# Kernel tuning notes

Measured on AMD Instinct MI355X. Metric: run time of the kernel, lower is better.

## Reference

```python
import jax, jax.numpy as jnp
import numpy as np
from jax import lax

D_MODEL = 1024
D_STATE = 16
D_CONV = 4
D_INNER = 2048  # expand * d_model
DT_RANK = 64    # ceil(d_model / 16)
BATCH = 2
SEQ = 2048


def setup_inputs() -> dict:
    key = jax.random.key(0)
    ks = jax.random.split(key, 8)
    s = 0.02
    x = jax.random.normal(ks[0], (BATCH, SEQ, D_MODEL), jnp.float32)
    in_proj_w = jax.random.normal(ks[1], (2 * D_INNER, D_MODEL), jnp.float32) * s
    conv_w = jax.random.normal(ks[2], (D_INNER, 1, D_CONV), jnp.float32) * s  # [out, in/groups, k]
    conv_b = jax.random.normal(ks[3], (D_INNER,), jnp.float32) * s
    x_proj_w = jax.random.normal(ks[4], (DT_RANK + 2 * D_STATE, D_INNER), jnp.float32) * s
    dt_proj_w = jax.random.normal(ks[5], (D_INNER, DT_RANK), jnp.float32) * s
    dt_proj_b = jax.random.normal(ks[6], (D_INNER,), jnp.float32) * s
    A_log = jnp.log(jnp.tile(jnp.arange(1, D_STATE + 1, dtype=jnp.float32), (D_INNER, 1)))
    D = jnp.ones((D_INNER,), jnp.float32)
    out_proj_w = jax.random.normal(ks[7], (D_MODEL, D_INNER), jnp.float32) * s
    return dict(x=x, in_proj_w=in_proj_w, conv_w=conv_w, conv_b=conv_b,
                x_proj_w=x_proj_w, dt_proj_w=dt_proj_w, dt_proj_b=dt_proj_b,
                A_log=A_log, D=D, out_proj_w=out_proj_w)


def _causal_depthwise_conv(x_bcl, conv_w, conv_b):
    # x_bcl: [B, d_inner, L]; conv_w: [d_inner, 1, k]; left-pad k-1 -> causal, output length L
    y = lax.conv_general_dilated(
        x_bcl, conv_w,
        window_strides=(1,), padding=[(D_CONV - 1, 0)],
        feature_group_count=D_INNER,
        dimension_numbers=('NCH', 'OIH', 'NCH'))
    return y + conv_b[None, :, None]


def _ssm(xc, x_proj_w, dt_proj_w, dt_proj_b, A_log, D):
    # xc: [B, L, d_inner]
    A = -jnp.exp(A_log)                                   # [d, N]
    x_dbl = jnp.einsum('bld,rd->blr', xc, x_proj_w)       # [B, L, dt_rank + 2N]
    dt_low = x_dbl[..., :DT_RANK]
    Bm = x_dbl[..., DT_RANK:DT_RANK + D_STATE]            # [B, L, N]
    Cm = x_dbl[..., DT_RANK + D_STATE:]                   # [B, L, N]
    dt = jax.nn.softplus(jnp.einsum('blr,dr->bld', dt_low, dt_proj_w) + dt_proj_b)  # [B, L, d]
    dA = jnp.exp(dt[..., None] * A)                       # [B, L, d, N]
    dBx = dt[..., None] * Bm[:, :, None, :] * xc[..., None]  # [B, L, d, N]

    def step(h, inp):
        dA_t, dBx_t, C_t = inp                            # [B,d,N], [B,d,N], [B,N]
        h = dA_t * h + dBx_t
        y = jnp.einsum('bdn,bn->bd', h, C_t)
        return h, y

    h0 = jnp.zeros((xc.shape[0], D_INNER, D_STATE), xc.dtype)
    _, ys = lax.scan(step, h0,
                     (dA.transpose(1, 0, 2, 3), dBx.transpose(1, 0, 2, 3), Cm.transpose(1, 0, 2)))
    y = ys.transpose(1, 0, 2)                             # [B, L, d]
    return y + xc * D


def reference(x, in_proj_w, conv_w, conv_b, x_proj_w, dt_proj_w, dt_proj_b, A_log, D, out_proj_w):
    xz = jnp.einsum('blm,om->blo', x, in_proj_w)          # [B, L, 2*d_inner]
    xs, z = jnp.split(xz, 2, axis=-1)
    xc = _causal_depthwise_conv(xs.transpose(0, 2, 1), conv_w, conv_b).transpose(0, 2, 1)
    xc = jax.nn.silu(xc)
    y = _ssm(xc, x_proj_w, dt_proj_w, dt_proj_b, A_log, D)
    out = y * jax.nn.silu(z)
    return jnp.einsum('bld,md->blm', out, out_proj_w)
```

## Files before the change

### kernel.cpp

```cpp
#include <hip/hip_runtime.h>

#define SEQ    2048
#define DIN    2048
#define DMODEL 1024
#define NROWS  4096
#define NCH    64
#define CHL    32

typedef __attribute__((ext_vector_type(8))) _Float16 half8v;
typedef __attribute__((ext_vector_type(8))) unsigned short ushort8v;
typedef __attribute__((ext_vector_type(4))) float f32x4;

__device__ __forceinline__ float sigf(float x) { return 1.0f / (1.0f + __expf(-x)); }
__device__ __forceinline__ float softplusf(float v) {
    return fmaxf(v, 0.f) + __logf(1.f + __expf(-fabsf(v)));
}

__device__ __forceinline__ void gload16(const void* g, const void* l) {
    __builtin_amdgcn_global_load_lds((const __attribute__((address_space(1))) void*)g,
                                     (__attribute__((address_space(3))) void*)l, 16, 0, 0);
}

__device__ __forceinline__ unsigned short f2h(float x) {
    _Float16 h = (_Float16)x;
    unsigned short u;
    __builtin_memcpy(&u, &h, 2);
    return u;
}
__device__ __forceinline__ float h2f(unsigned short u) {
    _Float16 h;
    __builtin_memcpy(&h, &u, 2);
    return (float)h;
}

__global__ __launch_bounds__(256) void cvt_in_k(
    const float* __restrict__ x, const float* __restrict__ wi, const float* __restrict__ wx,
    const float* __restrict__ wd, const float* __restrict__ wo,
    unsigned short* __restrict__ xh, unsigned short* __restrict__ wih,
    unsigned short* __restrict__ wxh, unsigned short* __restrict__ wdh,
    unsigned short* __restrict__ woh)
{
    int i = blockIdx.x * 256 + threadIdx.x;
    if (i < 1048576) {
        float4 v = ((const float4*)x)[i];
        ushort4 h; h.x = f2h(v.x); h.y = f2h(v.y); h.z = f2h(v.z); h.w = f2h(v.w);
        ((ushort4*)xh)[i] = h;
    } else if (i < 2097152) {
        i -= 1048576;
        float4 v = ((const float4*)wi)[i];
        ushort4 h; h.x = f2h(v.x); h.y = f2h(v.y); h.z = f2h(v.z); h.w = f2h(v.w);
        ((ushort4*)wih)[i] = h;
    } else if (i < 2162688) {
        i -= 2097152;
        int row = i >> 9, q = i & 511;
        ushort4 h;
        if (row < 96) {
            float4 v = ((const float4*)wx)[(size_t)row * 512 + q];
            h.x = f2h(v.x); h.y = f2h(v.y); h.z = f2h(v.z); h.w = f2h(v.w);
        } else h = make_ushort4(0, 0, 0, 0);
        ((ushort4*)wxh)[(size_t)row * 512 + q] = h;
    } else if (i < 2195456) {
        i -= 2162688;
        float4 v = ((const float4*)wd)[i];
        ushort4 h; h.x = f2h(v.x); h.y = f2h(v.y); h.z = f2h(v.z); h.w = f2h(v.w);
        ((ushort4*)wdh)[i] = h;
    } else {
        i -= 2195456;
        float4 v = ((const float4*)wo)[i];
        ushort4 h; h.x = f2h(v.x); h.y = f2h(v.y); h.z = f2h(v.z); h.w = f2h(v.w);
        ((ushort4*)woh)[i] = h;
    }
}

__global__ __launch_bounds__(512, 4) void gemm_inproj(
    const unsigned short* __restrict__ A, const unsigned short* __restrict__ W,
    unsigned short* __restrict__ C, int K, int N, int mtiles, int lda, int ldw)
{
    __shared__ uint4 ldsu4[3072];
    char* lds = (char*)ldsu4;
    const int tid = threadIdx.x;
    const int w = tid >> 6, lane = tid & 63;

    const int nwg = gridDim.x;
    const int cpx = nwg >> 3;
    const int bid = blockIdx.x;
    const int swz = (bid & 7) * cpx + (bid >> 3);
    const int ntiles = nwg / mtiles;
    const int per = 8 * ntiles;
    const int gid = swz / per;
    const int rem = swz - gid * per;
    const int m0 = (gid * 8 + (rem & 7)) * 256;
    const int n0 = (rem >> 3) * 128;

    const int wr = w >> 2, wc = w & 3;
    const int lm = lane & 15, lk = lane >> 4;

    f32x4 acc[8][2];
#pragma unroll
    for (int i = 0; i < 8; ++i)
#pragma unroll
        for (int j = 0; j < 2; ++j) { acc[i][j][0]=0.f; acc[i][j][1]=0.f; acc[i][j][2]=0.f; acc[i][j][3]=0.f; }

    const int rsub = w * 8 + (lane >> 3);
    const int xr8  = ((lane & 7) ^ (lane >> 3)) << 3;
    const unsigned short* gA = A + (size_t)(m0 + rsub) * lda + xr8;
    const unsigned short* gW = W + (size_t)(n0 + rsub) * ldw + xr8;
    const int sdst = w * 1024;

    for (int kt = 0; kt < K; kt += 64) {
#pragma unroll
        for (int i = 0; i < 4; ++i)
            gload16(gA + (size_t)i * 64 * lda + kt, lds + i * 8192 + sdst);
#pragma unroll
        for (int i = 0; i < 2; ++i)
            gload16(gW + (size_t)i * 64 * ldw + kt, lds + 32768 + i * 8192 + sdst);
        __syncthreads();
#pragma unroll
        for (int kk = 0; kk < 2; ++kk) {
            half8v b[2];
#pragma unroll
            for (int nb = 0; nb < 2; ++nb) {
                const int br = wc * 32 + nb * 16 + lm;
                b[nb] = *(const half8v*)(lds + 32768 + br * 128 + (((kk * 4 + lk) ^ (br & 7)) << 4));
            }
            __builtin_amdgcn_s_setprio(1);
#pragma unroll
            for (int mb = 0; mb < 8; ++mb) {
                const int ar = wr * 128 + mb * 16 + lm;
                half8v a = *(const half8v*)(lds + ar * 128 + (((kk * 4 + lk) ^ (ar & 7)) << 4));
#pragma unroll
                for (int nb = 0; nb < 2; ++nb)
                    acc[mb][nb] = __builtin_amdgcn_mfma_f32_16x16x32_f16(a, b[nb], acc[mb][nb], 0, 0, 0);
            }
            __builtin_amdgcn_s_setprio(0);
        }
        __syncthreads();
    }

#pragma unroll
    for (int mb = 0; mb < 8; ++mb)
#pragma unroll
        for (int nb = 0; nb < 2; ++nb)
#pragma unroll
            for (int r = 0; r < 4; ++r)
                C[(size_t)(m0 + wr * 128 + mb * 16 + lk * 4 + r) * N + (n0 + wc * 32 + nb * 16 + lm)]
                    = f2h(acc[mb][nb][r]);
}

#define A_OFF 0
#define W_OFF 16384

__global__ __launch_bounds__(256) void gemm_mfma_h(
    const unsigned short* __restrict__ A, const unsigned short* __restrict__ W,
    unsigned short* __restrict__ C, int K, int ldc, int nmax, int mtiles,
    int sA1, int sA2, int ldw, const float* __restrict__ bias, int kspl, int cstride)
{
    __shared__ uint4 ldsu4[2048];
    char* lds = (char*)ldsu4;
    const int tid  = threadIdx.x;
    const int w    = tid >> 6, lane = tid & 63;

    const int nwg = gridDim.x;
    const int cpx = nwg >> 3;
    const int bid = blockIdx.x;
    const int swz = (bid & 7) * cpx + (bid >> 3);
    const int nbp = nwg / kspl;
    const int ks  = swz / nbp;
    const int tt  = swz - ks * nbp;
    const int ntiles = nbp / mtiles;
    const int per = 8 * ntiles;
    const int gid = tt / per;
    const int rem = tt - gid * per;
    const int m0 = (gid * 8 + (rem & 7)) * 128;
    const int n0 = (rem >> 3) * 128;
    const int kOff = ks * K;

    const int wr = w >> 1, wc = w & 1;

    f32x4 acc[4][4];
#pragma unroll
    for (int i = 0; i < 4; ++i)
#pragma unroll
        for (int j = 0; j < 4; ++j) { acc[i][j][0]=0.f; acc[i][j][1]=0.f; acc[i][j][2]=0.f; acc[i][j][3]=0.f; }

    const int rloc = w * 32 + (lane >> 3);
    const int xr8  = ((lane & 7) ^ (lane >> 3)) << 3;
    const int rowA = m0 + rloc;
    const unsigned short* gA = A + (size_t)(rowA >> 1) * sA2 + (size_t)(rowA & 1) * sA1 + kOff + xr8;
    const unsigned short* gW = W + (size_t)(n0 + rloc) * ldw + kOff + xr8;

    const int lm  = lane & 15;
    const int lk  = lane >> 4;
    const int lk4 = lk * 4;

    for (int kt = 0; kt < K; kt += 64) {
#pragma unroll
        for (int i = 0; i < 4; ++i) {
            const int rb = w * 32 + i * 8;
            gload16(gA + (size_t)i * 4 * sA2 + kt, lds + A_OFF + rb * 128);
            gload16(gW + (size_t)i * 8 * ldw + kt, lds + W_OFF + rb * 128);
        }
        __syncthreads();
#pragma unroll
        for (int h = 0; h < 2; ++h) {
            half8v af[4], wf[4];
            const int ch = h * 4 + lk;
#pragma unroll
            for (int t = 0; t < 4; ++t) {
                const int ar = wr * 64 + t * 16 + lm;
                const int wrw = wc * 64 + t * 16 + lm;
                af[t] = *(const half8v*)(lds + A_OFF + ar * 128 + ((ch ^ (ar & 7)) << 4));
                wf[t] = *(const half8v*)(lds + W_OFF + wrw * 128 + ((ch ^ (wrw & 7)) << 4));
            }
#pragma unroll
            for (int i = 0; i < 4; ++i)
#pragma unroll
                for (int j = 0; j < 4; ++j)
                    acc[i][j] = __builtin_amdgcn_mfma_f32_16x16x32_f16(af[i], wf[j], acc[i][j], 0, 0, 0);
        }
        __syncthreads();
    }

    unsigned short* Cp = C + (size_t)ks * cstride;
    if (bias) {
#pragma unroll
        for (int j = 0; j < 4; ++j) {
            const int n = n0 + wc * 64 + j * 16 + lm;
            const float bv = (n < nmax) ? bias[n] : 0.f;
#pragma unroll
            for (int i = 0; i < 4; ++i)
#pragma unroll
                for (int r = 0; r < 4; ++r) {
                    float v = acc[i][j][r] + bv;
                    if (n < nmax)
                        Cp[(size_t)(m0 + wr * 64 + i * 16 + lk4 + r) * ldc + n] = f2h(softplusf(v));
                }
        }
    } else {
#pragma unroll
        for (int i = 0; i < 4; ++i)
#pragma unroll
            for (int j = 0; j < 4; ++j) {
                const int n = n0 + wc * 64 + j * 16 + lm;
                if (n < nmax)
#pragma unroll
                    for (int r = 0; r < 4; ++r)
                        Cp[(size_t)(m0 + wr * 64 + i * 16 + lk4 + r) * ldc + n] = f2h(acc[i][j][r]);
            }
    }
}

__global__ __launch_bounds__(256) void xproj_reduce_k(
    const unsigned short* __restrict__ part, float* __restrict__ xdbl,
    unsigned short* __restrict__ dlh)
{
    int i = blockIdx.x * 256 + threadIdx.x;
    if (i >= NROWS * 32) return;
    int row = i >> 5, q = i & 31;
    float s0 = 0.f, s1 = 0.f, s2 = 0.f, s3 = 0.f;
#pragma unroll
    for (int ks = 0; ks < 8; ++ks) {
        ushort4 v = *(const ushort4*)(part + (size_t)ks * (NROWS * 128) + (size_t)row * 128 + q * 4);
        s0 += h2f(v.x); s1 += h2f(v.y); s2 += h2f(v.z); s3 += h2f(v.w);
    }
    if (q < 16) {
        ushort4 h; h.x = f2h(s0); h.y = f2h(s1); h.z = f2h(s2); h.w = f2h(s3);
        *(ushort4*)(dlh + (size_t)row * 64 + q * 4) = h;
    } else {
        *(float4*)(xdbl + (size_t)row * 96 + q * 4) = make_float4(s0, s1, s2, s3);
    }
}

__global__ __launch_bounds__(256) void out_reduce_k(
    const unsigned short* __restrict__ p, float* __restrict__ out)
{
    int i = blockIdx.x * 256 + threadIdx.x;
    ushort4 a = ((const ushort4*)p)[i];
    ushort4 b = ((const ushort4*)(p + 4194304))[i];
    float4 v;
    v.x = h2f(a.x) + h2f(b.x);
    v.y = h2f(a.y) + h2f(b.y);
    v.z = h2f(a.z) + h2f(b.z);
    v.w = h2f(a.w) + h2f(b.w);
    ((float4*)out)[i] = v;
}

__global__ __launch_bounds__(256) void conv_silu_k(
    const unsigned short* __restrict__ xzh, const float* __restrict__ cw,
    const float* __restrict__ cb, unsigned short* __restrict__ xch)
{
    int i = blockIdx.x * 256 + threadIdx.x;
    int d8 = (i & 255) << 3;
    int row = i >> 8;
    int l = row & (SEQ - 1);
    const unsigned short* base = xzh + (size_t)row * 4096 + d8;
    ushort8v x0 = *(const ushort8v*)base;
    ushort8v x1 = {}, x2 = {}, x3 = {};
    if (l >= 1) x1 = *(const ushort8v*)(base - 4096);
    if (l >= 2) x2 = *(const ushort8v*)(base - 8192);
    if (l >= 3) x3 = *(const ushort8v*)(base - 12288);
    ushort8v out;
#pragma unroll
    for (int j = 0; j < 8; ++j) {
        float4 wv = *(const float4*)(cw + (size_t)(d8 + j) * 4);
        float a = cb[d8 + j];
        a = fmaf(h2f(x3[j]), wv.x, a);
        a = fmaf(h2f(x2[j]), wv.y, a);
        a = fmaf(h2f(x1[j]), wv.z, a);
        a = fmaf(h2f(x0[j]), wv.w, a);
        out[j] = f2h(a * sigf(a));
    }
    *(ushort8v*)(xch + (size_t)row * DIN + d8) = out;
}

__global__ __launch_bounds__(256) void scan_pass1(
    const unsigned short* __restrict__ dth, const unsigned short* __restrict__ xch,
    const float* __restrict__ xdbl, const float* __restrict__ Alog,
    float* __restrict__ hbuf, float* __restrict__ apbuf)
{
    const int b = blockIdx.z, c = blockIdx.y;
    const int d = blockIdx.x * 256 + threadIdx.x;
    float A[16];
#pragma unroll
    for (int q = 0; q < 4; ++q) *(float4*)&A[q * 4] = *(const float4*)&Alog[(size_t)d * 16 + q * 4];
    bool seq = true;
#pragma unroll
    for (int n = 0; n < 16; ++n) {
        A[n] = -__expf(A[n]);
        seq = seq && (fabsf(A[n] + (float)(n + 1)) < 1e-5f * (float)(n + 1));
    }
    float h[16] = {};
    float sumdt = 0.f;
    const int rowbase = b * SEQ + c * CHL;
    int row = rowbase;
    float dtv = h2f(dth[(size_t)row * DIN + d]);
    float xcv = h2f(xch[(size_t)row * DIN + d]);
    if (seq) {
        for (int t = 0; t < CHL; ++t) {
            const int nrow = row + ((t + 1) < CHL ? 1 : 0);
            float dtv2 = h2f(dth[(size_t)nrow * DIN + d]);
            float xcv2 = h2f(xch[(size_t)nrow * DIN + d]);
            const float* xr = xdbl + (size_t)row * 96;
            float u = dtv * xcv;
            sumdt += dtv;
            float r = __expf(-dtv);
            float dA = r;
#pragma unroll
            for (int n = 0; n < 16; ++n) {
                h[n] = fmaf(dA, h[n], u * xr[64 + n]);
                dA *= r;
            }
            dtv = dtv2; xcv = xcv2; row = nrow;
        }
    } else {
        for (int t = 0; t < CHL; ++t) {
            const int nrow = row + ((t + 1) < CHL ? 1 : 0);
            float dtv2 = h2f(dth[(size_t)nrow * DIN + d]);
            float xcv2 = h2f(xch[(size_t)nrow * DIN + d]);
            const float* xr = xdbl + (size_t)row * 96;
            float u = dtv * xcv;
            sumdt += dtv;
#pragma unroll
            for (int n = 0; n < 16; ++n) {
                float dA = __expf(dtv * A[n]);
                h[n] = fmaf(dA, h[n], u * xr[64 + n]);
            }
            dtv = dtv2; xcv = xcv2; row = nrow;
        }
    }
    float ap[16];
    if (seq) {
        float R = __expf(-sumdt);
        float a = R;
#pragma unroll
        for (int n = 0; n < 16; ++n) { ap[n] = a; a *= R; }
    } else {
#pragma unroll
        for (int n = 0; n < 16; ++n) ap[n] = __expf(sumdt * A[n]);
    }
    size_t e = ((size_t)(b * NCH + c) << 15) + (size_t)d * 16;
#pragma unroll
    for (int q = 0; q < 4; ++q) {
        *(float4*)(hbuf + e + q * 4)  = *(float4*)&h[q * 4];
        *(float4*)(apbuf + e + q * 4) = *(float4*)&ap[q * 4];
    }
}

__global__ __launch_bounds__(256) void scan_pass2(
    float* __restrict__ hbuf, const float* __restrict__ apbuf)
{
    int idx = blockIdx.x * 256 + threadIdx.x;
    int b = idx >> 15;
    int dn = idx & 32767;
    float carry = 0.f;
    for (int c = 0; c < NCH; ++c) {
        size_t e = ((size_t)(b * NCH + c) << 15) + dn;
        float hl = hbuf[e];
        float ap = apbuf[e];
        hbuf[e] = carry;
        carry = fmaf(ap, carry, hl);
    }
}

__global__ __launch_bounds__(256) void scan_pass3(
    const unsigned short* __restrict__ dth, const unsigned short* __restrict__ xch,
    const unsigned short* __restrict__ xzh, const float* __restrict__ xdbl,
    const float* __restrict__ Alog, const float* __restrict__ Dp,
    const float* __restrict__ hbuf, unsigned short* __restrict__ oph)
{
    const int b = blockIdx.z, c = blockIdx.y;
    const int d = blockIdx.x * 256 + threadIdx.x;
    float A[16];
#pragma unroll
    for (int q = 0; q < 4; ++q) *(float4*)&A[q * 4] = *(const float4*)&Alog[(size_t)d * 16 + q * 4];
    bool seq = true;
#pragma unroll
    for (int n = 0; n < 16; ++n) {
        A[n] = -__expf(A[n]);
        seq = seq && (fabsf(A[n] + (float)(n + 1)) < 1e-5f * (float)(n + 1));
    }
    float h[16];
    size_t e = ((size_t)(b * NCH + c) << 15) + (size_t)d * 16;
#pragma unroll
    for (int q = 0; q < 4; ++q) *(float4*)&h[q * 4] = *(const float4*)(hbuf + e + q * 4);
    const float Dd = Dp[d];
    const int rowbase = b * SEQ + c * CHL;
    int row = rowbase;
    float dtv = h2f(dth[(size_t)row * DIN + d]);
    float xcv = h2f(xch[(size_t)row * DIN + d]);
    float zv  = h2f(xzh[(size_t)row * 4096 + DIN + d]);
    if (seq) {
        for (int t = 0; t < CHL; ++t) {
            const int nrow = row + ((t + 1) < CHL ? 1 : 0);
            float dtv2 = h2f(dth[(size_t)nrow * DIN + d]);
            float xcv2 = h2f(xch[(size_t)nrow * DIN + d]);
            float zv2  = h2f(xzh[(size_t)nrow * 4096 + DIN + d]);
            const float* xr = xdbl + (size_t)row * 96;
            float u = dtv * xcv;
            float r = __expf(-dtv);
            float dA = r;
            float y = 0.f;
#pragma unroll
            for (int n = 0; n < 16; ++n) {
                h[n] = fmaf(dA, h[n], u * xr[64 + n]);
                y = fmaf(h[n], xr[80 + n], y);
                dA *= r;
            }
            float val = (y + xcv * Dd) * zv * sigf(zv);
            oph[(size_t)row * DIN + d] = f2h(val);
            dtv = dtv2; xcv = xcv2; zv = zv2; row = nrow;
        }
    } else {
        for (int t = 0; t < CHL; ++t) {
            const int nrow = row + ((t + 1) < CHL ? 1 : 0);
            float dtv2 = h2f(dth[(size_t)nrow * DIN + d]);
            float xcv2 = h2f(xch[(size_t)nrow * DIN + d]);
            float zv2  = h2f(xzh[(size_t)nrow * 4096 + DIN + d]);
            const float* xr = xdbl + (size_t)row * 96;
            float u = dtv * xcv;
            float y = 0.f;
#pragma unroll
            for (int n = 0; n < 16; ++n) {
                float dA = __expf(dtv * A[n]);
                h[n] = fmaf(dA, h[n], u * xr[64 + n]);
                y = fmaf(h[n], xr[80 + n], y);
            }
            float val = (y + xcv * Dd) * zv * sigf(zv);
            oph[(size_t)row * DIN + d] = f2h(val);
            dtv = dtv2; xcv = xcv2; zv = zv2; row = nrow;
        }
    }
}

extern "C" void kernel_launch(void* const* d_in, const int* in_sizes, int n_in,
                              void* d_out, int out_size, void* d_ws, size_t ws_size,
                              hipStream_t stream)
{
    const float* x    = (const float*)d_in[0];
    const float* wi   = (const float*)d_in[1];
    const float* cw   = (const float*)d_in[2];
    const float* cb   = (const float*)d_in[3];
    const float* wx   = (const float*)d_in[4];
    const float* wd   = (const float*)d_in[5];
    const float* bd   = (const float*)d_in[6];
    const float* alog = (const float*)d_in[7];
    const float* Dp   = (const float*)d_in[8];
    const float* wo   = (const float*)d_in[9];
    float* out = (float*)d_out;

    float* wsf  = (float*)d_ws;
    float* xzr  = wsf;
    float* xcr  = wsf + 16777216;
    float* xdbl = wsf + 25165824;
    float* dtr  = wsf + 25559040;

    unsigned short* xzh = (unsigned short*)xzr;
    float* scr = xzr + 8388608;
    unsigned short* oph = (unsigned short*)scr;
    float* hbuf         = scr + 4194304;

    unsigned short* xh  = (unsigned short*)xcr;
    unsigned short* xch = (unsigned short*)xcr;
    float* apbuf        = xcr + 4194304;

    unsigned short* wih    = (unsigned short*)dtr;
    unsigned short* dth    = (unsigned short*)dtr;
    unsigned short* oparth = (unsigned short*)dtr;
    unsigned short* wxh    = (unsigned short*)(dtr + 4194304);
    unsigned short* xparth = (unsigned short*)(dtr + 4325376);
    unsigned short* woh    = (unsigned short*)(dtr + 6422528);
    unsigned short* wdh    = (unsigned short*)(dtr + 7471104);
    unsigned short* dlh    = (unsigned short*)(dtr + 7536640);

    cvt_in_k<<<10624, 256, 0, stream>>>(x, wi, wx, wd, wo, xh, wih, wxh, wdh, woh);
    gemm_inproj<<<512, 512, 0, stream>>>(xh, wih, xzh, 1024, 4096, 16, 1024, 1024);
    conv_silu_k<<<4096, 256, 0, stream>>>(xzh, cw, cb, xch);
    gemm_mfma_h<<<256, 256, 0, stream>>>(xch, wxh, xparth, 256, 128, 128, 32, 2048, 4096, 2048,
                                         nullptr, 8, NROWS * 128);
    xproj_reduce_k<<<512, 256, 0, stream>>>(xparth, xdbl, dlh);
    gemm_mfma_h<<<512, 256, 0, stream>>>(dlh, wdh, dth, 64, 2048, 2048, 32, 64, 128, 64,
                                         bd, 1, 0);
    scan_pass1<<<dim3(8, NCH, 2), 256, 0, stream>>>(dth, xch, xdbl, alog, hbuf, apbuf);
    scan_pass2<<<256, 256, 0, stream>>>(hbuf, apbuf);
    scan_pass3<<<dim3(8, NCH, 2), 256, 0, stream>>>(dth, xch, xzh, xdbl, alog, Dp, hbuf, oph);
    gemm_mfma_h<<<512, 256, 0, stream>>>(oph, woh, oparth, 1024, 1024, 1024, 32, 2048, 4096, 2048,
                                         nullptr, 2, 4194304);
    out_reduce_k<<<4096, 256, 0, stream>>>(oparth, out);
}
```

Baseline: 196.1 us.

## Halve scan chunk count and store chunk states in fp16

Doubles the scan chunk length so there are half as many chunks, and stores per-chunk hidden states and decay products as fp16 instead of fp32. This cuts the traffic of the chunked-scan carry buffers and shortens the sequential carry pass. The trade-off is fewer parallel blocks in the two per-chunk passes, longer serial loops per thread, and reduced precision of the cross-chunk states, which can underflow or lose accuracy.

```diff
diff --git a/kernel.cpp b/kernel.cpp
--- a/kernel.cpp
+++ b/kernel.cpp
@@ -4,8 +4,8 @@
 #define DIN    2048
 #define DMODEL 1024
 #define NROWS  4096
-#define NCH    64
-#define CHL    32
+#define NCH    32
+#define CHL    64
 
 typedef __attribute__((ext_vector_type(8))) _Float16 half8v;
 typedef __attribute__((ext_vector_type(8))) unsigned short ushort8v;
@@ -316,7 +316,7 @@
 __global__ __launch_bounds__(256) void scan_pass1(
     const unsigned short* __restrict__ dth, const unsigned short* __restrict__ xch,
     const float* __restrict__ xdbl, const float* __restrict__ Alog,
-    float* __restrict__ hbuf, float* __restrict__ apbuf)
+    unsigned short* __restrict__ hbuf, unsigned short* __restrict__ apbuf)
 {
     const int b = blockIdx.z, c = blockIdx.y;
     const int d = blockIdx.x * 256 + threadIdx.x;
@@ -379,15 +379,20 @@
         for (int n = 0; n < 16; ++n) ap[n] = __expf(sumdt * A[n]);
     }
     size_t e = ((size_t)(b * NCH + c) << 15) + (size_t)d * 16;
-#pragma unroll
-    for (int q = 0; q < 4; ++q) {
-        *(float4*)(hbuf + e + q * 4)  = *(float4*)&h[q * 4];
-        *(float4*)(apbuf + e + q * 4) = *(float4*)&ap[q * 4];
-    }
+    ushort8v hv0, hv1, av0, av1;
+#pragma unroll
+    for (int n = 0; n < 8; ++n) {
+        hv0[n] = f2h(h[n]);  hv1[n] = f2h(h[8 + n]);
+        av0[n] = f2h(ap[n]); av1[n] = f2h(ap[8 + n]);
+    }
+    *(ushort8v*)(hbuf + e)      = hv0;
+    *(ushort8v*)(hbuf + e + 8)  = hv1;
+    *(ushort8v*)(apbuf + e)     = av0;
+    *(ushort8v*)(apbuf + e + 8) = av1;
 }
 
 __global__ __launch_bounds__(256) void scan_pass2(
-    float* __restrict__ hbuf, const float* __restrict__ apbuf)
+    unsigned short* __restrict__ hbuf, const unsigned short* __restrict__ apbuf)
 {
     int idx = blockIdx.x * 256 + threadIdx.x;
     int b = idx >> 15;
@@ -395,9 +400,9 @@
     float carry = 0.f;
     for (int c = 0; c < NCH; ++c) {
         size_t e = ((size_t)(b * NCH + c) << 15) + dn;
-        float hl = hbuf[e];
-        float ap = apbuf[e];
-        hbuf[e] = carry;
+        float hl = h2f(hbuf[e]);
+        float ap = h2f(apbuf[e]);
+        hbuf[e] = f2h(carry);
         carry = fmaf(ap, carry, hl);
     }
 }
@@ -406,7 +411,7 @@
     const unsigned short* __restrict__ dth, const unsigned short* __restrict__ xch,
     const unsigned short* __restrict__ xzh, const float* __restrict__ xdbl,
     const float* __restrict__ Alog, const float* __restrict__ Dp,
-    const float* __restrict__ hbuf, unsigned short* __restrict__ oph)
+    const unsigned short* __restrict__ hbuf, unsigned short* __restrict__ oph)
 {
     const int b = blockIdx.z, c = blockIdx.y;
     const int d = blockIdx.x * 256 + threadIdx.x;
@@ -421,8 +426,12 @@
     }
     float h[16];
     size_t e = ((size_t)(b * NCH + c) << 15) + (size_t)d * 16;
-#pragma unroll
-    for (int q = 0; q < 4; ++q) *(float4*)&h[q * 4] = *(const float4*)(hbuf + e + q * 4);
+    {
+        ushort8v hv0 = *(const ushort8v*)(hbuf + e);
+        ushort8v hv1 = *(const ushort8v*)(hbuf + e + 8);
+#pragma unroll
+        for (int n = 0; n < 8; ++n) { h[n] = h2f(hv0[n]); h[8 + n] = h2f(hv1[n]); }
+    }
     const float Dd = Dp[d];
     const int rowbase = b * SEQ + c * CHL;
     int row = rowbase;
@@ -496,12 +505,12 @@
 
     unsigned short* xzh = (unsigned short*)xzr;
     float* scr = xzr + 8388608;
-    unsigned short* oph = (unsigned short*)scr;
-    float* hbuf         = scr + 4194304;
-
-    unsigned short* xh  = (unsigned short*)xcr;
-    unsigned short* xch = (unsigned short*)xcr;
-    float* apbuf        = xcr + 4194304;
+    unsigned short* oph  = (unsigned short*)scr;
+    unsigned short* hbuf = (unsigned short*)(scr + 4194304);
+
+    unsigned short* xh    = (unsigned short*)xcr;
+    unsigned short* xch   = (unsigned short*)xcr;
+    unsigned short* apbuf = (unsigned short*)(xcr + 4194304);
 
     unsigned short* wih    = (unsigned short*)dtr;
     unsigned short* dth    = (unsigned short*)dtr;
```

Measured after the change: 198.2 us. No clear change (+1.1%).
